# Kernel tuning notes

Measured on AMD Instinct MI355X. Metric: run time of the kernel, lower is better.

The kernel has to match this reference:

```python
import jax, jax.numpy as jnp
import numpy as np

N, E, H, ED = 20000, 640000, 128, 16


def _lin_init(k, fan_in, fan_out):
    kw, kb = jax.random.split(k)
    lim = 1.0 / np.sqrt(fan_in)
    W = jax.random.uniform(kw, (fan_in, fan_out), jnp.float32, -lim, lim)
    b = jax.random.uniform(kb, (fan_out,), jnp.float32, -lim, lim)
    return W, b


def setup_inputs() -> dict:
    key = jax.random.key(0)
    ks = jax.random.split(key, 12)
    h = jax.random.normal(ks[0], (N, H), jnp.float32)
    x = jax.random.normal(ks[1], (N, 3), jnp.float32)
    edge_index = jax.random.randint(ks[2], (2, E), 0, N, jnp.int32)
    edge_attr = jax.random.normal(ks[3], (E, ED), jnp.float32)
    fixed_mask = jax.random.randint(ks[4], (N,), 0, 2, jnp.int32).astype(bool)
    We1, be1 = _lin_init(ks[5], 2 * H + 1 + ED, H)
    We2, be2 = _lin_init(ks[6], H, H)
    Wx1, bx1 = _lin_init(ks[7], H, H)
    Wx2, bx2 = _lin_init(ks[8], H, 1)
    Wh1, bh1 = _lin_init(ks[9], 2 * H, H)
    Wh2, bh2 = _lin_init(ks[10], H, H)
    return {"h": h, "x": x, "edge_index": edge_index, "edge_attr": edge_attr,
            "fixed_mask": fixed_mask,
            "We1": We1, "be1": be1, "We2": We2, "be2": be2,
            "Wx1": Wx1, "bx1": bx1, "Wx2": Wx2, "bx2": bx2,
            "Wh1": Wh1, "bh1": bh1, "Wh2": Wh2, "bh2": bh2}


def reference(h, x, edge_index, edge_attr, fixed_mask,
              We1, be1, We2, be2, Wx1, bx1, Wx2, bx2, Wh1, bh1, Wh2, bh2):
    src, dst = edge_index[0], edge_index[1]
    n = h.shape[0]
    diff = x[src] - x[dst]                               # [E,3]
    dist_sq_norm = jnp.sum(diff * diff, -1, keepdims=True) / 100.0
    e_in = jnp.concatenate([h[src], h[dst], dist_sq_norm, edge_attr], -1)
    m_ij = jax.nn.silu(jax.nn.silu(e_in @ We1 + be1) @ We2 + be2)  # [E,H]
    coord_w = jnp.tanh(jax.nn.silu(m_ij @ Wx1 + bx1) @ Wx2 + bx2)  # [E,1]
    coord_agg = jax.ops.segment_sum(diff * coord_w, dst, num_segments=n)
    coord_agg = coord_agg * (~fixed_mask).astype(h.dtype)[:, None]
    msg_agg = jax.ops.segment_sum(m_ij, dst, num_segments=n)       # [N,H]
    h_new = h + jax.nn.silu(jnp.concatenate([h, msg_agg], -1) @ Wh1 + bh1) @ Wh2 + bh2
    x_new = x + coord_agg
    return h_new, x_new
```

## Files before the change

kernel.cpp:

```cpp
#include <hip/hip_runtime.h>
#include <hip/hip_bf16.h>
#include <math.h>

#define NN   20000
#define NE   640000
#define HD   128
#define EDIM 16
#define KIN  273
#define P2   136

#define S_PWT   4096
#define S_PWE1M 32768
#define S_PW4   16384
#define S_PWH1  32768
#define S_PWH2  16384

typedef __bf16 bf16x8 __attribute__((ext_vector_type(8)));
typedef float  f32x4  __attribute__((ext_vector_type(4)));

__device__ __forceinline__ float silu_f(float v) {
    const float e = __expf(-v);
    return v * __builtin_amdgcn_rcpf(1.0f + e);
}
__device__ __forceinline__ float tanh_f(float s) {
    const float e = __expf(2.0f * s);
    return 1.0f - 2.0f * __builtin_amdgcn_rcpf(e + 1.0f);
}
__device__ __forceinline__ unsigned short f2bf(float f) {
    __bf16 b = (__bf16)f;
    return __builtin_bit_cast(unsigned short, b);
}
__device__ __forceinline__ float bf2f(unsigned short u) {
    __bf16 b = __builtin_bit_cast(__bf16, u);
    return (float)b;
}
__device__ __forceinline__ unsigned pack2bf(float a, float b) {
    return (unsigned)f2bf(a) | ((unsigned)f2bf(b) << 16);
}
__device__ __forceinline__ bf16x8 ldcvt_bf8(const float* __restrict__ p) {
    const float4 v0 = ((const float4*)p)[0];
    const float4 v1 = ((const float4*)p)[1];
    bf16x8 av;
    av[0]=(__bf16)v0.x; av[1]=(__bf16)v0.y; av[2]=(__bf16)v0.z; av[3]=(__bf16)v0.w;
    av[4]=(__bf16)v1.x; av[5]=(__bf16)v1.y; av[6]=(__bf16)v1.z; av[7]=(__bf16)v1.w;
    return av;
}

__device__ __forceinline__ void pack_id(const float* __restrict__ W, int Kreal,
                                        unsigned short* __restrict__ P, int idx) {
    const int f = idx >> 9, r = idx & 511;
    const int lane = r >> 3, j = r & 7;
    const int kb = f >> 3, nb = f & 7;
    const int k = kb * 32 + (lane >> 4) * 8 + j;
    const int n = nb * 16 + (lane & 15);
    P[idx] = f2bf((k < Kreal) ? W[(size_t)k * HD + n] : 0.0f);
}
__device__ __forceinline__ void pack_il(const float* __restrict__ W, int Kreal,
                                        unsigned short* __restrict__ P, int idx) {
    const int f = idx >> 9, r = idx & 511;
    const int lane = r >> 3, j = r & 7;
    const int kb = f >> 3, nb = f & 7;
    const int k = kb * 32 + (lane >> 4) * 8 + j;
    const int n = (nb >> 1) * 32 + 2 * (lane & 15) + (nb & 1);
    P[idx] = f2bf((k < Kreal) ? W[(size_t)k * HD + n] : 0.0f);
}


__global__ void egnn_prep_kernel(
    const int* __restrict__ ei,
    const float* __restrict__ We1, const float* __restrict__ We2,
    const float* __restrict__ Wx1, const float* __restrict__ Wh1,
    const float* __restrict__ Wh2,
    unsigned short* __restrict__ PWt,  unsigned short* __restrict__ PWe1m,
    unsigned short* __restrict__ PWe2, unsigned short* __restrict__ PWx1,
    unsigned short* __restrict__ PWh1, unsigned short* __restrict__ PWh2,
    int* __restrict__ cnt)
{
    const size_t T1 = S_PWT, T2 = T1 + S_PWE1M, T3 = T2 + S_PW4;
    const size_t T4 = T3 + S_PW4, T5 = T4 + S_PWH1, T6 = T5 + S_PWH2;
    const size_t TOT = T6 + NE;
    const size_t stride = (size_t)gridDim.x * blockDim.x;
    for (size_t i = (size_t)blockIdx.x * blockDim.x + threadIdx.x; i < TOT; i += stride) {
        if (i < T1) {
            const int idx = (int)i;
            const int r = idx & 511, nb = idx >> 9;
            const int lane = r >> 3, j = r & 7;
            const int k = 256 + (lane >> 4) * 8 + j;
            const int n = (nb >> 1) * 32 + 2 * (lane & 15) + (nb & 1);
            PWt[idx] = f2bf((k < KIN) ? We1[(size_t)k * HD + n] : 0.0f);
            continue;
        }
        if (i < T2) { pack_il(We1, 256, PWe1m, (int)(i - T1)); continue; }
        if (i < T3) { pack_il(We2, HD, PWe2, (int)(i - T2)); continue; }
        if (i < T4) { pack_il(Wx1, HD, PWx1, (int)(i - T3)); continue; }
        if (i < T5) { pack_id(Wh1, 2 * HD, PWh1, (int)(i - T4)); continue; }
        if (i < T6) { pack_id(Wh2, HD, PWh2, (int)(i - T5)); continue; }
        atomicAdd(&cnt[ei[NE + (i - T6)]], 1);
    }
}

__global__ __launch_bounds__(256, 4) void egnn_pre_kernel(
    const float* __restrict__ h,
    const unsigned short* __restrict__ PWe1m, const float* __restrict__ be1,
    const int* __restrict__ cnt, int* __restrict__ cursor,
    unsigned short* __restrict__ preS, unsigned short* __restrict__ preD)
{
    const int t = threadIdx.x;
    if (blockIdx.x == 625) {
        __shared__ int ls[256];
        const int base = t * 79;
        int c[79];
        int s = 0;
        for (int i = 0; i < 79; ++i) {
            const int idx = base + i;
            c[i] = (idx < NN) ? cnt[idx] : 0;
            s += c[i];
        }
        ls[t] = s;
        __syncthreads();
        int v = s;
        for (int off = 1; off < 256; off <<= 1) {
            const int u = (t >= off) ? ls[t - off] : 0;
            __syncthreads();
            v += u;
            ls[t] = v;
            __syncthreads();
        }
        int run = v - s;
        for (int i = 0; i < 79; ++i) {
            const int idx = base + i;
            if (idx < NN) { cursor[idx] = run; run += c[i]; }
        }
        return;
    }
    const int n0 = blockIdx.x * 32;
    const int lane = t & 63, w = t >> 6;
    const int quad = lane >> 4, l16 = lane & 15;
    int arow[2];
    #pragma unroll
    for (int mb = 0; mb < 2; ++mb) arow[mb] = min(n0 + mb * 16 + l16, NN - 1);

    f32x4 accS[2][2], accD[2][2];
    #pragma unroll
    for (int mb = 0; mb < 2; ++mb)
        #pragma unroll
        for (int nt = 0; nt < 2; ++nt) {
            accS[mb][nt] = (f32x4){0.f,0.f,0.f,0.f};
            accD[mb][nt] = (f32x4){0.f,0.f,0.f,0.f};
        }
    #pragma unroll
    for (int kb = 0; kb < 4; ++kb) {
        bf16x8 a[2], bS[2], bD[2];
        #pragma unroll
        for (int mb = 0; mb < 2; ++mb)
            a[mb] = ldcvt_bf8(&h[(size_t)arow[mb] * HD + kb * 32 + quad * 8]);
        #pragma unroll
        for (int nt = 0; nt < 2; ++nt) {
            bS[nt] = *(const bf16x8*)&PWe1m[((kb * 8 + w * 2 + nt) * 64 + lane) * 8];
            bD[nt] = *(const bf16x8*)&PWe1m[(((4 + kb) * 8 + w * 2 + nt) * 64 + lane) * 8];
        }
        #pragma unroll
        for (int mb = 0; mb < 2; ++mb)
            #pragma unroll
            for (int nt = 0; nt < 2; ++nt) {
                accS[mb][nt] = __builtin_amdgcn_mfma_f32_16x16x32_bf16(
                    a[mb], bS[nt], accS[mb][nt], 0, 0, 0);
                accD[mb][nt] = __builtin_amdgcn_mfma_f32_16x16x32_bf16(
                    a[mb], bD[nt], accD[mb][nt], 0, 0, 0);
            }
    }
    const int cb = w * 32 + 2 * l16;
    const float2 b1 = *(const float2*)&be1[cb];
    #pragma unroll
    for (int mb = 0; mb < 2; ++mb)
        #pragma unroll
        for (int r = 0; r < 4; ++r) {
            const int n = n0 + mb * 16 + quad * 4 + r;
            if (n < NN) {
                *(unsigned*)&preS[(size_t)n * HD + cb] =
                    pack2bf(accS[mb][0][r], accS[mb][1][r]);
                *(unsigned*)&preD[(size_t)n * HD + cb] =
                    pack2bf(accD[mb][0][r] + b1.x, accD[mb][1][r] + b1.y);
            }
        }
}

__global__ void egnn_perm_kernel(const int* __restrict__ ei,
                                 int* __restrict__ cursor, int* __restrict__ perm) {
    const int e = blockIdx.x * 256 + threadIdx.x;
    const int pos = atomicAdd(&cursor[ei[NE + e]], 1);
    perm[pos] = e;
}

__global__ __launch_bounds__(256, 6) void egnn_edge_kernel(
    const unsigned short* __restrict__ preS, const unsigned short* __restrict__ preD,
    const float* __restrict__ x,
    const int* __restrict__ ei, const float* __restrict__ eattr,
    const int* __restrict__ perm,
    const unsigned short* __restrict__ PWt,
    const unsigned short* __restrict__ PWe2, const float* __restrict__ be2,
    const unsigned short* __restrict__ PWx1, const float* __restrict__ bx1,
    const float* __restrict__ Wx2, const float* __restrict__ bx2,
    float* __restrict__ msg_agg, float* __restrict__ coord_agg)
{
    __shared__ __align__(16) unsigned short buf[64 * P2];
    __shared__ int   sE[64], sSrc[64], sDst[64];
    __shared__ float sDiff[64][3];
    __shared__ float sW[64];

    const int t  = threadIdx.x;
    const int e0 = blockIdx.x * 64;
    unsigned short* tail = buf;

    if (t < 64) {
        const int e = perm[e0 + t];
        sE[t] = e;
        const int s = ei[e];
        const int d = ei[NE + e];
        sSrc[t] = s; sDst[t] = d;
        const float dx = x[s*3+0] - x[d*3+0];
        const float dy = x[s*3+1] - x[d*3+1];
        const float dz = x[s*3+2] - x[d*3+2];
        sDiff[t][0] = dx; sDiff[t][1] = dy; sDiff[t][2] = dz;
        tail[t * 32 + 0] = f2bf((dx*dx + dy*dy + dz*dz) * 0.01f);
    }
    __syncthreads();

    const int lane = t & 63;
    const int w    = t >> 6;
    const int quad = lane >> 4;
    const int l16  = lane & 15;
    const int cb   = w * 32 + 2 * l16;

    f32x4 preC[4][2];
    #pragma unroll
    for (int mb = 0; mb < 4; ++mb)
        #pragma unroll
        for (int r = 0; r < 4; ++r) {
            const int row = mb * 16 + quad * 4 + r;
            const unsigned us = *(const unsigned*)&preS[(size_t)sSrc[row] * HD + cb];
            const unsigned ud = *(const unsigned*)&preD[(size_t)sDst[row] * HD + cb];
            preC[mb][0][r] = bf2f((unsigned short)(us & 0xffff)) +
                             bf2f((unsigned short)(ud & 0xffff));
            preC[mb][1][r] = bf2f((unsigned short)(us >> 16)) +
                             bf2f((unsigned short)(ud >> 16));
        }

    {
        const int eL = t >> 2, q = t & 3;
        const int eG = sE[eL];
        #pragma unroll
        for (int jj = 0; jj < 8; ++jj) {
            const int col = q * 8 + jj;
            if (col == 0) continue;
            float v = 0.0f;
            if (col <= EDIM) v = eattr[(size_t)eG * EDIM + (col - 1)];
            tail[eL * 32 + col] = f2bf(v);
        }
    }
    __syncthreads();

    f32x4 acc1[4][2];
    {
        bf16x8 a[4], b[2];
        #pragma unroll
        for (int mb = 0; mb < 4; ++mb)
            a[mb] = *(const bf16x8*)&tail[(mb * 16 + l16) * 32 + quad * 8];
        #pragma unroll
        for (int nt = 0; nt < 2; ++nt)
            b[nt] = *(const bf16x8*)&PWt[((w * 2 + nt) * 64 + lane) * 8];
        #pragma unroll
        for (int mb = 0; mb < 4; ++mb)
            #pragma unroll
            for (int nt = 0; nt < 2; ++nt)
                acc1[mb][nt] = __builtin_amdgcn_mfma_f32_16x16x32_bf16(
                    a[mb], b[nt], preC[mb][nt], 0, 0, 0);
    }
    __syncthreads();

    #pragma unroll
    for (int mb = 0; mb < 4; ++mb)
        #pragma unroll
        for (int r = 0; r < 4; ++r) {
            const int row = mb * 16 + quad * 4 + r;
            *(unsigned*)&buf[row * P2 + cb] =
                pack2bf(silu_f(acc1[mb][0][r]), silu_f(acc1[mb][1][r]));
        }
    __syncthreads();

    const float2 b2 = *(const float2*)&be2[cb];
    f32x4 acc2[4][2];
    #pragma unroll
    for (int mb = 0; mb < 4; ++mb) {
        acc2[mb][0] = (f32x4){b2.x, b2.x, b2.x, b2.x};
        acc2[mb][1] = (f32x4){b2.y, b2.y, b2.y, b2.y};
    }
    #pragma unroll
    for (int kb = 0; kb < 4; ++kb) {
        bf16x8 a[4], b[2];
        #pragma unroll
        for (int mb = 0; mb < 4; ++mb)
            a[mb] = *(const bf16x8*)&buf[(mb * 16 + l16) * P2 + kb * 32 + quad * 8];
        #pragma unroll
        for (int nt = 0; nt < 2; ++nt)
            b[nt] = *(const bf16x8*)&PWe2[((kb * 8 + w * 2 + nt) * 64 + lane) * 8];
        #pragma unroll
        for (int mb = 0; mb < 4; ++mb)
            #pragma unroll
            for (int nt = 0; nt < 2; ++nt)
                acc2[mb][nt] = __builtin_amdgcn_mfma_f32_16x16x32_bf16(
                    a[mb], b[nt], acc2[mb][nt], 0, 0, 0);
    }
    __syncthreads();

    {
        #pragma unroll
        for (int mb = 0; mb < 4; ++mb)
            #pragma unroll
            for (int r = 0; r < 4; ++r) {
                const int row = mb * 16 + quad * 4 + r;
                *(unsigned*)&buf[row * P2 + cb] =
                    pack2bf(silu_f(acc2[mb][0][r]),
                            silu_f(acc2[mb][1][r]));
            }
    }
    __syncthreads();

    {
        const int cp = t & 63;
        const int r0 = (t >> 6) * 16;
        float a0 = 0.0f, a1 = 0.0f;
        #pragma unroll 4
        for (int r = 0; r < 16; ++r) {
            const int row = r0 + r;
            const int d   = sDst[row];
            const unsigned u = *(const unsigned*)&buf[row * P2 + 2 * cp];
            a0 += bf2f((unsigned short)(u & 0xffff));
            a1 += bf2f((unsigned short)(u >> 16));
            const bool flush = (r == 15) || (sDst[row + 1] != d);
            if (flush) {
                atomicAdd(&msg_agg[(size_t)d * HD + 2 * cp], a0);
                atomicAdd(&msg_agg[(size_t)d * HD + 2 * cp + 1], a1);
                a0 = 0.0f; a1 = 0.0f;
            }
        }
    }

    const float2 bx = *(const float2*)&bx1[cb];
    const float2 w2 = *(const float2*)&Wx2[cb];
    f32x4 acc3[4][2];
    #pragma unroll
    for (int mb = 0; mb < 4; ++mb) {
        acc3[mb][0] = (f32x4){bx.x, bx.x, bx.x, bx.x};
        acc3[mb][1] = (f32x4){bx.y, bx.y, bx.y, bx.y};
    }
    #pragma unroll
    for (int kb = 0; kb < 4; ++kb) {
        bf16x8 a[4], b[2];
        #pragma unroll
        for (int mb = 0; mb < 4; ++mb)
            a[mb] = *(const bf16x8*)&buf[(mb * 16 + l16) * P2 + kb * 32 + quad * 8];
        #pragma unroll
        for (int nt = 0; nt < 2; ++nt)
            b[nt] = *(const bf16x8*)&PWx1[((kb * 8 + w * 2 + nt) * 64 + lane) * 8];
        #pragma unroll
        for (int mb = 0; mb < 4; ++mb)
            #pragma unroll
            for (int nt = 0; nt < 2; ++nt)
                acc3[mb][nt] = __builtin_amdgcn_mfma_f32_16x16x32_bf16(
                    a[mb], b[nt], acc3[mb][nt], 0, 0, 0);
    }
    float p[4][4];
    {
        #pragma unroll
        for (int mb = 0; mb < 4; ++mb)
            #pragma unroll
            for (int r = 0; r < 4; ++r)
                p[mb][r] = silu_f(acc3[mb][0][r]) * w2.x +
                           silu_f(acc3[mb][1][r]) * w2.y;
        #pragma unroll
        for (int off = 8; off >= 1; off >>= 1)
            #pragma unroll
            for (int mb = 0; mb < 4; ++mb)
                #pragma unroll
                for (int r = 0; r < 4; ++r)
                    p[mb][r] += __shfl_xor(p[mb][r], off, 64);
    }
    __syncthreads();

    if (l16 == 0) {
        float* red = reinterpret_cast<float*>(buf);
        #pragma unroll
        for (int mb = 0; mb < 4; ++mb)
            #pragma unroll
            for (int r = 0; r < 4; ++r)
                red[w * 64 + mb * 16 + quad * 4 + r] = p[mb][r];
    }
    __syncthreads();
    if (t < 64) {
        const float* red = reinterpret_cast<const float*>(buf);
        sW[t] = tanh_f(red[t] + red[64 + t] + red[128 + t] + red[192 + t] + bx2[0]);
    }
    __syncthreads();

    if (w < 3) {
        const int dstv = sDst[lane];
        float v = sDiff[lane][w] * sW[lane];
        #pragma unroll
        for (int off = 1; off <= 32; off <<= 1) {
            const int   dn = __shfl_down(dstv, off, 64);
            const float vn = __shfl_down(v, off, 64);
            if (lane + off < 64 && dn == dstv) v += vn;
        }
        const int up = __shfl_up(dstv, 1, 64);
        if (lane == 0 || up != dstv)
            atomicAdd(&coord_agg[(size_t)dstv * 3 + w], v);
    }
}

__global__ __launch_bounds__(256, 4) void egnn_node_kernel(
    const float* __restrict__ h,
    const float* __restrict__ x, const int* __restrict__ fixed_mask,
    const unsigned short* __restrict__ PWh1, const float* __restrict__ bh1,
    const unsigned short* __restrict__ PWh2, const float* __restrict__ bh2,
    const float* __restrict__ msg_agg, const float* __restrict__ coord_agg,
    float* __restrict__ out_h, float* __restrict__ out_x)
{
    __shared__ __align__(16) unsigned short sTn[32 * P2];
    const int t  = threadIdx.x;
    const int n0 = blockIdx.x * 32;
    const int lane = t & 63, w = t >> 6;
    const int quad = lane >> 4, l16 = lane & 15;

    if (t < 96) {
        const int ln = t / 3, d3 = t - ln * 3;
        const int n  = n0 + ln;
        if (n < NN) {
            const float add = (fixed_mask[n] != 0) ? 0.0f : coord_agg[(size_t)n*3 + d3];
            out_x[(size_t)n*3 + d3] = x[(size_t)n*3 + d3] + add;
        }
    }

    int nrow[2];
    #pragma unroll
    for (int mb = 0; mb < 2; ++mb) nrow[mb] = min(n0 + mb * 16 + l16, NN - 1);

    f32x4 acc[2][2];
    #pragma unroll
    for (int nt = 0; nt < 2; ++nt) {
        const float bias = bh1[w * 32 + nt * 16 + l16];
        #pragma unroll
        for (int mb = 0; mb < 2; ++mb)
            acc[mb][nt] = (f32x4){bias, bias, bias, bias};
    }

    #pragma unroll
    for (int kb = 0; kb < 8; ++kb) {
        bf16x8 a[2], b[2];
        if (kb < 4) {
            #pragma unroll
            for (int mb = 0; mb < 2; ++mb)
                a[mb] = ldcvt_bf8(&h[(size_t)nrow[mb] * HD + kb * 32 + quad * 8]);
        } else {
            #pragma unroll
            for (int mb = 0; mb < 2; ++mb)
                a[mb] = ldcvt_bf8(&msg_agg[(size_t)nrow[mb] * HD + (kb - 4) * 32 + quad * 8]);
        }
        #pragma unroll
        for (int nt = 0; nt < 2; ++nt)
            b[nt] = *(const bf16x8*)&PWh1[((kb * 8 + w * 2 + nt) * 64 + lane) * 8];
        #pragma unroll
        for (int mb = 0; mb < 2; ++mb)
            #pragma unroll
            for (int nt = 0; nt < 2; ++nt)
                acc[mb][nt] = __builtin_amdgcn_mfma_f32_16x16x32_bf16(
                    a[mb], b[nt], acc[mb][nt], 0, 0, 0);
    }
    #pragma unroll
    for (int nt = 0; nt < 2; ++nt) {
        const int col = w * 32 + nt * 16 + l16;
        #pragma unroll
        for (int mb = 0; mb < 2; ++mb)
            #pragma unroll
            for (int r = 0; r < 4; ++r) {
                const int row = mb * 16 + quad * 4 + r;
                sTn[row * P2 + col] = f2bf(silu_f(acc[mb][nt][r]));
            }
    }
    __syncthreads();

    #pragma unroll
    for (int nt = 0; nt < 2; ++nt) {
        const float bias = bh2[w * 32 + nt * 16 + l16];
        #pragma unroll
        for (int mb = 0; mb < 2; ++mb)
            acc[mb][nt] = (f32x4){bias, bias, bias, bias};
    }
    #pragma unroll
    for (int kb = 0; kb < 4; ++kb) {
        bf16x8 a[2], b[2];
        #pragma unroll
        for (int mb = 0; mb < 2; ++mb)
            a[mb] = *(const bf16x8*)&sTn[(mb * 16 + l16) * P2 + kb * 32 + quad * 8];
        #pragma unroll
        for (int nt = 0; nt < 2; ++nt)
            b[nt] = *(const bf16x8*)&PWh2[((kb * 8 + w * 2 + nt) * 64 + lane) * 8];
        #pragma unroll
        for (int mb = 0; mb < 2; ++mb)
            #pragma unroll
            for (int nt = 0; nt < 2; ++nt)
                acc[mb][nt] = __builtin_amdgcn_mfma_f32_16x16x32_bf16(
                    a[mb], b[nt], acc[mb][nt], 0, 0, 0);
    }
    #pragma unroll
    for (int nt = 0; nt < 2; ++nt) {
        const int col = w * 32 + nt * 16 + l16;
        #pragma unroll
        for (int mb = 0; mb < 2; ++mb)
            #pragma unroll
            for (int r = 0; r < 4; ++r) {
                const int row = mb * 16 + quad * 4 + r;
                const int n   = n0 + row;
                if (n < NN)
                    out_h[(size_t)n * HD + col] =
                        h[(size_t)n * HD + col] + acc[mb][nt][r];
            }
    }
}

extern "C" void kernel_launch(void* const* d_in, const int* in_sizes, int n_in,
                              void* d_out, int out_size, void* d_ws, size_t ws_size,
                              hipStream_t stream)
{
    const float* h     = (const float*)d_in[0];
    const float* x     = (const float*)d_in[1];
    const int*   ei    = (const int*)d_in[2];
    const float* eattr = (const float*)d_in[3];
    const int*   fmask = (const int*)d_in[4];
    const float* We1   = (const float*)d_in[5];
    const float* be1   = (const float*)d_in[6];
    const float* We2   = (const float*)d_in[7];
    const float* be2   = (const float*)d_in[8];
    const float* Wx1   = (const float*)d_in[9];
    const float* bx1   = (const float*)d_in[10];
    const float* Wx2   = (const float*)d_in[11];
    const float* bx2   = (const float*)d_in[12];
    const float* Wh1   = (const float*)d_in[13];
    const float* bh1   = (const float*)d_in[14];
    const float* Wh2   = (const float*)d_in[15];
    const float* bh2   = (const float*)d_in[16];

    float* msg    = (float*)d_ws;
    float* coord  = msg + (size_t)NN * HD;
    int*   cnt    = (int*)(coord + (size_t)NN * 3);
    int*   cursor = cnt + NN;
    int*   perm   = cursor + NN;
    unsigned short* preS  = (unsigned short*)(perm + NE);
    unsigned short* preD  = preS + (size_t)NN * HD;
    unsigned short* PWt   = preD + (size_t)NN * HD;
    unsigned short* PWe1m = PWt + S_PWT;
    unsigned short* PWe2  = PWe1m + S_PWE1M;
    unsigned short* PWx1  = PWe2 + S_PW4;
    unsigned short* PWh1  = PWx1 + S_PW4;
    unsigned short* PWh2  = PWh1 + S_PWH1;

    float* out_h = (float*)d_out;
    float* out_x = out_h + (size_t)NN * HD;

    hipMemsetAsync(d_ws, 0, (size_t)NN * (HD + 4) * sizeof(int), stream);
    egnn_prep_kernel<<<1024, 256, 0, stream>>>(
        ei, We1, We2, Wx1, Wh1, Wh2,
        PWt, PWe1m, PWe2, PWx1, PWh1, PWh2, cnt);
    egnn_pre_kernel<<<626, 256, 0, stream>>>(h, PWe1m, be1, cnt, cursor, preS, preD);
    egnn_perm_kernel<<<NE / 256, 256, 0, stream>>>(ei, cursor, perm);
    egnn_edge_kernel<<<NE / 64, 256, 0, stream>>>(
        preS, preD, x, ei, eattr, perm, PWt, PWe2, be2, PWx1, bx1,
        Wx2, bx2, msg, coord);
    egnn_node_kernel<<<(NN + 31) / 32, 256, 0, stream>>>(
        h, x, fmask, PWh1, bh1, PWh2, bh2, msg, coord, out_h, out_x);
}
```

Measured before the change: 378.4 us.

## Scatter src/dst pairs and bf16 edge attributes into sorted order during permutation

The permutation kernel now writes each edge's (src,dst) pair and its edge attributes, converted to bf16, directly into destination-sorted positions. The edge kernel can then read them contiguously instead of following perm to gather from ei and eattr. The weight tail is reordered so the 16 edge-attribute columns come first and the distance term sits at column 16, which lets the tile be filled with two aligned 16-byte loads per edge. This removes one __syncthreads and the scattered fp32 eattr reads from the edge kernel. In exchange it adds a bf16 staging buffer of E×16 values, and the perm kernel now does a scattered write of that buffer.

Result: faster. 365.9 us, median of 2 (-3.3%).

```diff
diff --git a/kernel.cpp b/kernel.cpp
--- a/kernel.cpp
+++ b/kernel.cpp
@@ -85,9 +85,12 @@
             const int idx = (int)i;
             const int r = idx & 511, nb = idx >> 9;
             const int lane = r >> 3, j = r & 7;
-            const int k = 256 + (lane >> 4) * 8 + j;
+            const int kk = (lane >> 4) * 8 + j;
             const int n = (nb >> 1) * 32 + 2 * (lane & 15) + (nb & 1);
-            PWt[idx] = f2bf((k < KIN) ? We1[(size_t)k * HD + n] : 0.0f);
+            int wr = -1;
+            if (kk < 16) wr = 257 + kk;
+            else if (kk == 16) wr = 256;
+            PWt[idx] = f2bf((wr >= 0) ? We1[(size_t)wr * HD + n] : 0.0f);
             continue;
         }
         if (i < T2) { pack_il(We1, 256, PWe1m, (int)(i - T1)); continue; }
@@ -186,17 +189,32 @@
 }
 
 __global__ void egnn_perm_kernel(const int* __restrict__ ei,
-                                 int* __restrict__ cursor, int* __restrict__ perm) {
+                                 const float* __restrict__ eattr,
+                                 int* __restrict__ cursor,
+                                 int2* __restrict__ sdP,
+                                 unsigned short* __restrict__ eattrB) {
     const int e = blockIdx.x * 256 + threadIdx.x;
-    const int pos = atomicAdd(&cursor[ei[NE + e]], 1);
-    perm[pos] = e;
+    const int s = ei[e];
+    const int d = ei[NE + e];
+    const int pos = atomicAdd(&cursor[d], 1);
+    sdP[pos] = make_int2(s, d);
+    const float4 v0 = ((const float4*)eattr)[(size_t)e * 4 + 0];
+    const float4 v1 = ((const float4*)eattr)[(size_t)e * 4 + 1];
+    const float4 v2 = ((const float4*)eattr)[(size_t)e * 4 + 2];
+    const float4 v3 = ((const float4*)eattr)[(size_t)e * 4 + 3];
+    uint4 a, b;
+    a.x = pack2bf(v0.x, v0.y); a.y = pack2bf(v0.z, v0.w);
+    a.z = pack2bf(v1.x, v1.y); a.w = pack2bf(v1.z, v1.w);
+    b.x = pack2bf(v2.x, v2.y); b.y = pack2bf(v2.z, v2.w);
+    b.z = pack2bf(v3.x, v3.y); b.w = pack2bf(v3.z, v3.w);
+    ((uint4*)eattrB)[(size_t)pos * 2 + 0] = a;
+    ((uint4*)eattrB)[(size_t)pos * 2 + 1] = b;
 }
 
 __global__ __launch_bounds__(256, 6) void egnn_edge_kernel(
     const unsigned short* __restrict__ preS, const unsigned short* __restrict__ preD,
     const float* __restrict__ x,
-    const int* __restrict__ ei, const float* __restrict__ eattr,
-    const int* __restrict__ perm,
+    const int2* __restrict__ sdP, const unsigned short* __restrict__ eattrB,
     const unsigned short* __restrict__ PWt,
     const unsigned short* __restrict__ PWe2, const float* __restrict__ be2,
     const unsigned short* __restrict__ PWx1, const float* __restrict__ bx1,
@@ -204,7 +222,7 @@
     float* __restrict__ msg_agg, float* __restrict__ coord_agg)
 {
     __shared__ __align__(16) unsigned short buf[64 * P2];
-    __shared__ int   sE[64], sSrc[64], sDst[64];
+    __shared__ int   sSrc[64], sDst[64];
     __shared__ float sDiff[64][3];
     __shared__ float sW[64];
 
@@ -213,16 +231,27 @@
     unsigned short* tail = buf;
 
     if (t < 64) {
-        const int e = perm[e0 + t];
-        sE[t] = e;
-        const int s = ei[e];
-        const int d = ei[NE + e];
+        const int2 sd = sdP[e0 + t];
+        const int s = sd.x, d = sd.y;
         sSrc[t] = s; sDst[t] = d;
         const float dx = x[s*3+0] - x[d*3+0];
         const float dy = x[s*3+1] - x[d*3+1];
         const float dz = x[s*3+2] - x[d*3+2];
         sDiff[t][0] = dx; sDiff[t][1] = dy; sDiff[t][2] = dz;
-        tail[t * 32 + 0] = f2bf((dx*dx + dy*dy + dz*dz) * 0.01f);
+        tail[t * 32 + 16] = f2bf((dx*dx + dy*dy + dz*dz) * 0.01f);
+    }
+    {
+        const int eL = t >> 2, q = t & 3;
+        if (q < 2) {
+            const uint4 v = ((const uint4*)eattrB)[(size_t)(e0 + eL) * 2 + q];
+            *(uint4*)&tail[eL * 32 + q * 8] = v;
+        } else if (q == 2) {
+            #pragma unroll
+            for (int c = 17; c < 24; ++c) tail[eL * 32 + c] = 0;
+        } else {
+            #pragma unroll
+            for (int c = 24; c < 32; ++c) tail[eL * 32 + c] = 0;
+        }
     }
     __syncthreads();
 
@@ -245,20 +274,6 @@
             preC[mb][1][r] = bf2f((unsigned short)(us >> 16)) +
                              bf2f((unsigned short)(ud >> 16));
         }
-
-    {
-        const int eL = t >> 2, q = t & 3;
-        const int eG = sE[eL];
-        #pragma unroll
-        for (int jj = 0; jj < 8; ++jj) {
-            const int col = q * 8 + jj;
-            if (col == 0) continue;
-            float v = 0.0f;
-            if (col <= EDIM) v = eattr[(size_t)eG * EDIM + (col - 1)];
-            tail[eL * 32 + col] = f2bf(v);
-        }
-    }
-    __syncthreads();
 
     f32x4 acc1[4][2];
     {
@@ -554,8 +569,9 @@
     float* coord  = msg + (size_t)NN * HD;
     int*   cnt    = (int*)(coord + (size_t)NN * 3);
     int*   cursor = cnt + NN;
-    int*   perm   = cursor + NN;
-    unsigned short* preS  = (unsigned short*)(perm + NE);
+    int2*  sdP    = (int2*)(cursor + NN);
+    unsigned short* eattrB = (unsigned short*)(sdP + NE);
+    unsigned short* preS  = eattrB + (size_t)NE * 16;
     unsigned short* preD  = preS + (size_t)NN * HD;
     unsigned short* PWt   = preD + (size_t)NN * HD;
     unsigned short* PWe1m = PWt + S_PWT;
@@ -572,9 +588,9 @@
         ei, We1, We2, Wx1, Wh1, Wh2,
         PWt, PWe1m, PWe2, PWx1, PWh1, PWh2, cnt);
     egnn_pre_kernel<<<626, 256, 0, stream>>>(h, PWe1m, be1, cnt, cursor, preS, preD);
-    egnn_perm_kernel<<<NE / 256, 256, 0, stream>>>(ei, cursor, perm);
+    egnn_perm_kernel<<<NE / 256, 256, 0, stream>>>(ei, eattr, cursor, sdP, eattrB);
     egnn_edge_kernel<<<NE / 64, 256, 0, stream>>>(
-        preS, preD, x, ei, eattr, perm, PWt, PWe2, be2, PWx1, bx1,
+        preS, preD, x, sdP, eattrB, PWt, PWe2, be2, PWx1, bx1,
         Wx2, bx2, msg, coord);
     egnn_node_kernel<<<(NN + 31) / 32, 256, 0, stream>>>(
         h, x, fmask, PWh1, bh1, PWh2, bh2, msg, coord, out_h, out_x);
```
